# Kernel optimization log

Hardware: AMD Instinct MI355X
Metric: run time of the kernel (lower is better)

The kernel has to match this reference:

```python
import jax, jax.numpy as jnp
import numpy as np

NTOKEN, NINP, NHID, B = 32000, 1024, 1024, 4096


def _rev_lstm_cell(x, c, h, W, b):
    # W: [6, H, D_in+H], b: [6, H]. Gates 0..2 use concat(x,h); 3..5 use concat(x,new_c).
    cat1 = jnp.concatenate([x, h], axis=-1)                      # [B, D+H]
    z1 = jnp.einsum('bd,khd->bkh', cat1, W[:3]) + b[:3]          # [B, 3, H]
    f = jax.nn.sigmoid(z1[:, 0])
    i = jax.nn.sigmoid(z1[:, 1])
    c_ = jnp.tanh(z1[:, 2])
    new_c = (f * c + i * c_) * 0.5
    cat2 = jnp.concatenate([x, new_c], axis=-1)
    z2 = jnp.einsum('bd,khd->bkh', cat2, W[3:]) + b[3:]          # [B, 3, H]
    u = jax.nn.sigmoid(z2[:, 0])
    r = jax.nn.sigmoid(z2[:, 1])
    h_ = jnp.tanh(z2[:, 2])
    new_h = (r * h + u * h_) * 0.5
    return new_h, new_c


def setup_inputs() -> dict:
    key = jax.random.key(0)
    ks = jax.random.split(key, 8)
    gain = 0.01
    def xav(k, shape):
        fan_out, fan_in = shape[-2], shape[-1]
        a = gain * np.sqrt(6.0 / (fan_in + fan_out))
        return jax.random.uniform(k, shape, jnp.float32, -a, a)
    return {
        'input_ids': jax.random.randint(ks[0], (B,), 0, NTOKEN),
        'c1': jnp.zeros((B, NHID), jnp.float32),
        'h1': jnp.zeros((B, NHID), jnp.float32),
        'c2': jnp.zeros((B, NHID), jnp.float32),
        'h2': jnp.zeros((B, NHID), jnp.float32),
        'emb_W': jax.random.uniform(ks[1], (NTOKEN, NINP), jnp.float32, -0.1, 0.1),
        'cell1_W': xav(ks[2], (6, NHID, NINP + NHID)),
        'cell1_b': jnp.zeros((6, NHID), jnp.float32),
        'cell2_W': xav(ks[3], (6, NHID, NHID + NHID)),
        'cell2_b': jnp.zeros((6, NHID), jnp.float32),
        'dec_W': jax.random.uniform(ks[4], (NTOKEN, NHID), jnp.float32, -0.1, 0.1),
        'dec_b': jnp.zeros((NTOKEN,), jnp.float32),
    }


def reference(input_ids, c1, h1, c2, h2, emb_W, cell1_W, cell1_b, cell2_W, cell2_b, dec_W, dec_b):
    emb = emb_W[input_ids]                                       # [B, NINP]
    h1n, c1n = _rev_lstm_cell(emb, c1, h1, cell1_W, cell1_b)
    h2n, c2n = _rev_lstm_cell(h1n, c2, h2, cell2_W, cell2_b)
    decoded = h2n @ dec_W.T + dec_b                              # [B, NTOKEN]
    return decoded, c1n, h1n, c2n, h2n
```

## Files before the change

### kernel.cpp

```cpp
#include <hip/hip_runtime.h>


typedef __attribute__((ext_vector_type(4))) float f32x4;
typedef __attribute__((ext_vector_type(8))) short bf16x8;
typedef __attribute__((ext_vector_type(4))) unsigned short u16x4;
typedef __attribute__((ext_vector_type(4))) int i32x4;

__device__ __forceinline__ unsigned short f2bf(float x) {
  unsigned u = __float_as_uint(x);
  return (unsigned short)((u + 0x7fffu + ((u >> 16) & 1u)) >> 16);
}
__device__ __forceinline__ u16x4 cvt4v(f32x4 v) {
  u16x4 h;
  h[0] = f2bf(v[0]); h[1] = f2bf(v[1]); h[2] = f2bf(v[2]); h[3] = f2bf(v[3]);
  return h;
}
__device__ __forceinline__ float sigf(float x) { return 1.0f / (1.0f + expf(-x)); }

__device__ __forceinline__ void conv_chunk(const float* __restrict__ src,
                                           unsigned short* __restrict__ dst,
                                           long i, long n4) {
  if (i >= n4) return;
  f32x4 v = __builtin_nontemporal_load(reinterpret_cast<const f32x4*>(src) + i);
  reinterpret_cast<u16x4*>(dst)[i] = cvt4v(v);
}

__global__ void fused_pre(const float* __restrict__ W1, unsigned short* __restrict__ cWb1,
                          const float* __restrict__ W2, unsigned short* __restrict__ cWb2,
                          const int* __restrict__ ids, const float* __restrict__ embW,
                          const float* __restrict__ h1, const float* __restrict__ h2,
                          unsigned short* __restrict__ A0, unsigned short* __restrict__ A1,
                          unsigned short* __restrict__ A2) {
  const long n4 = 6L * 1024 * 2048 / 4;
  int b = blockIdx.x;
  int t = threadIdx.x;
  if (b < 12288) {
    conv_chunk(W1, cWb1, (long)b * 256 + t, n4);
  } else if (b < 24576) {
    conv_chunk(W2, cWb2, (long)(b - 12288) * 256 + t, n4);
  } else {
    int r = b - 24576;
    long erow = (long)ids[r] * 1024;
    u16x4 e = cvt4v(reinterpret_cast<const f32x4*>(embW + erow)[t]);
    reinterpret_cast<u16x4*>(A0 + (long)r * 2048)[t] = e;
    reinterpret_cast<u16x4*>(A1 + (long)r * 2048)[t] = e;
    reinterpret_cast<u16x4*>(A0 + (long)r * 2048 + 1024)[t] =
        cvt4v(reinterpret_cast<const f32x4*>(h1 + (long)r * 1024)[t]);
    reinterpret_cast<u16x4*>(A2 + (long)r * 2048 + 1024)[t] =
        cvt4v(reinterpret_cast<const f32x4*>(h2 + (long)r * 1024)[t]);
  }
}

__global__ void quantRow(const float* __restrict__ src, signed char* __restrict__ q,
                         float* __restrict__ scale) {
  int row = blockIdx.x * 4 + (threadIdx.x >> 6);
  int l = threadIdx.x & 63;
  const f32x4* p = reinterpret_cast<const f32x4*>(src + (long)row * 1024);
  f32x4 v[4];
  float m = 0.0f;
#pragma unroll
  for (int i = 0; i < 4; ++i) {
    v[i] = p[l * 4 + i];
#pragma unroll
    for (int j = 0; j < 4; ++j) m = fmaxf(m, fabsf(v[i][j]));
  }
#pragma unroll
  for (int off = 32; off > 0; off >>= 1) m = fmaxf(m, __shfl_xor(m, off));
  float s = (m > 0.0f) ? m * (1.0f / 127.0f) : 1.0f;
  if (l == 0) scale[row] = s;
  float inv = 1.0f / s;
  i32x4 w;
#pragma unroll
  for (int i = 0; i < 4; ++i) {
    int b0 = __float2int_rn(v[i][0] * inv);
    int b1 = __float2int_rn(v[i][1] * inv);
    int b2 = __float2int_rn(v[i][2] * inv);
    int b3 = __float2int_rn(v[i][3] * inv);
    b0 = min(127, max(-127, b0)); b1 = min(127, max(-127, b1));
    b2 = min(127, max(-127, b2)); b3 = min(127, max(-127, b3));
    w[i] = (b0 & 0xff) | ((b1 & 0xff) << 8) | ((b2 & 0xff) << 16) | (b3 << 24);
  }
  *reinterpret_cast<i32x4*>(q + (long)row * 1024 + l * 16) = w;
}

__device__ __forceinline__ void load16(const void* g, void* l) {
  __builtin_amdgcn_global_load_lds((const __attribute__((address_space(1))) unsigned int*)g,
                                   (__attribute__((address_space(3))) unsigned int*)l,
                                   16, 0, 0);
}

#define WAITV(n) do { asm volatile("s_waitcnt vmcnt(" #n ")" ::: "memory");      \
    __builtin_amdgcn_sched_barrier(0); } while (0)
#define BAR() __builtin_amdgcn_s_barrier()
#define SCHED0() __builtin_amdgcn_sched_barrier(0)

__device__ __forceinline__ void superblock(int gx, int gy, int& bx, int& by) {
  const int nwg = gx * gy;
  int bid = blockIdx.y * gx + blockIdx.x;
  const int q = nwg >> 3;
  const int x = bid & 7, j = bid >> 3;
  const int p = x >> 1, half = x & 1;
  const int w0 = (gx + 1) >> 1;
  int byl;
  if ((w0 << 2) == q) {
    bx = half * w0 + (j >> 2);
    byl = j & 3;
  } else {
    if (j < q - 2) { bx = (half ? w0 : 0) + (j >> 2); byl = j & 3; }
    else { bx = w0 - 1; byl = (half ? 2 : 0) + (j - (q - 2)); }
  }
  by = p * 4 + byl;
}

template <int SWAP>
__global__ __launch_bounds__(512, 2) void gemm8f(
    const unsigned short* __restrict__ A,
    const unsigned short* __restrict__ B,
    const float* __restrict__ bias,
    const float* __restrict__ prev,
    float* __restrict__ outf,
    unsigned short* __restrict__ obf1,
    unsigned short* __restrict__ obf2, long obld) {
  __shared__ unsigned short lds[57344];

  int bx, by;
  superblock(gridDim.x, gridDim.y, bx, by);
  const long m0 = (long)by * 256;

  const int tid = threadIdx.x;
  const int lane = tid & 63;
  const int wave = tid >> 6;
  const int wr = wave >> 2;
  const int wc = wave & 3;
  const int lr = lane & 15;
  const int lq = lane >> 4;
  const int kb = lq * 16;

  const int o0 = tid * 16, o1 = tid * 16 + 8192;
  const int q0 = o0 ^ (((o0 >> 7) & 3) << 4);
  const int q1 = o1 ^ (((o1 >> 7) & 3) << 4);
  const char* pa0 = (const char*)(A + (m0 + (q0 >> 6)) * 2048) + (q0 & 63);
  const char* pa1 = (const char*)(A + (m0 + (q1 >> 6)) * 2048) + (q1 & 63);
  const int oB1 = 8192 + (tid & 255) * 16;
  const int qB1 = oB1 ^ (((oB1 >> 7) & 3) << 4);
  const int lrow0 = q0 >> 6, lrow1 = qB1 >> 6;
  const long grow0 = (long)(lrow0 >> 6) * 1024 + bx * 64 + (lrow0 & 63);
  const long grow1 = (long)(lrow1 >> 6) * 1024 + bx * 64 + (lrow1 & 63);
  const char* pb0 = (const char*)(B + grow0 * 2048) + (q0 & 63);
  const char* pb1 = (const char*)(B + grow1 * 2048) + (qB1 & 63);

  const int NT = 32;

#define STG_A(t_, kh_) do { int ko = ((t_) << 7) + ((kh_) << 6);                 \
    char* base_ = (char*)&lds[0] + ((t_) & 1) * 57344;                           \
    char* dst = base_ + ((kh_) ? 28672 : 0);                                     \
    load16(pa0 + ko, dst + o0); load16(pa1 + ko, dst + o1); } while (0)
#define STG_B(t_, kh_) do { int ko = ((t_) << 7) + ((kh_) << 6);                 \
    char* base_ = (char*)&lds[0] + ((t_) & 1) * 57344;                           \
    char* dst = base_ + ((kh_) ? 45056 : 16384);                                 \
    load16(pb0 + ko, dst + o0); load16(pb1 + ko, dst + oB1); } while (0)
#define RDA(dst, bp, soff, ih) do {                                              \
    _Pragma("unroll") for (int i_ = 0; i_ < 4; ++i_) {                           \
      int o_ = (wr * 128 + ((ih) * 4 + i_) * 16 + lr) * 64 + kb;                 \
      o_ ^= ((o_ >> 7) & 3) << 4;                                                \
      dst[i_] = *(const bf16x8*)((bp) + (soff) + o_); } } while (0)
#define RDB(dst, bp, soff) do {                                                  \
    _Pragma("unroll") for (int g_ = 0; g_ < 3; ++g_) {                           \
      int o_ = (g_ * 64 + wc * 16 + lr) * 64 + kb;                               \
      o_ ^= ((o_ >> 7) & 3) << 4;                                                \
      dst[g_] = *(const bf16x8*)((bp) + (soff) + o_); } } while (0)
#define MF12(ar, af_, bf_) do {                                                  \
    _Pragma("unroll") for (int i_ = 0; i_ < 4; ++i_)                             \
    _Pragma("unroll") for (int g_ = 0; g_ < 3; ++g_)                             \
      acc[(ar) + i_][g_] = __builtin_amdgcn_mfma_f32_16x16x32_bf16(              \
          af_[i_], bf_[g_], acc[(ar) + i_][g_], 0, 0, 0); } while (0)

  f32x4 acc[8][3] = {};
  bf16x8 af1[4], af2[4], bfA[3], bfB[3];

  STG_B(0, 0); STG_A(0, 0); STG_B(0, 1); STG_A(0, 1);
  STG_B(1, 0); STG_A(1, 0); STG_B(1, 1);
  WAITV(10);
  BAR();
  {
    const char* b0 = (const char*)&lds[0];
    RDA(af1, b0, 0, 0);
    RDB(bfA, b0, 16384);
  }

  for (int t = 0; t < NT; ++t) {
    const char* base = (const char*)&lds[0] + (t & 1) * 57344;
    const char* baseN = (const char*)&lds[0] + ((t + 1) & 1) * 57344;
    RDA(af2, base, 0, 1);
    if (t + 1 < NT) STG_A(t + 1, 1);
    SCHED0();
    __builtin_amdgcn_s_setprio(1);
    MF12(0, af1, bfA);
    __builtin_amdgcn_s_setprio(0);
    if (t < NT - 1) { WAITV(8); } else { WAITV(0); }
    BAR();
    RDA(af1, base, 28672, 0);
    RDB(bfB, base, 45056);
    if (t + 2 < NT) STG_B(t + 2, 0);
    SCHED0();
    __builtin_amdgcn_s_setprio(1);
    MF12(4, af2, bfA);
    __builtin_amdgcn_s_setprio(0);
    BAR();
    RDA(af2, base, 28672, 1);
    if (t + 2 < NT) STG_A(t + 2, 0);
    SCHED0();
    __builtin_amdgcn_s_setprio(1);
    MF12(0, af1, bfB);
    __builtin_amdgcn_s_setprio(0);
    if (t < NT - 2) { WAITV(8); } else if (t == NT - 2) { WAITV(4); }
    BAR();
    if (t + 1 < NT) {
      RDA(af1, baseN, 0, 0);
      RDB(bfA, baseN, 16384);
    }
    if (t + 2 < NT) STG_B(t + 2, 1);
    SCHED0();
    __builtin_amdgcn_s_setprio(1);
    MF12(4, af2, bfB);
    __builtin_amdgcn_s_setprio(0);
    BAR();
  }

  const long colg = (long)bx * 64 + wc * 16 + lr;
  const float b0v = bias[colg];
  const float b1v = bias[1024 + colg];
  const float b2v = bias[2048 + colg];
#pragma unroll
  for (int i = 0; i < 8; ++i) {
#pragma unroll
    for (int qq = 0; qq < 4; ++qq) {
      long r = m0 + wr * 128 + i * 16 + lq * 4 + qq;
      float z0 = acc[i][0][qq] + b0v;
      float z1 = acc[i][1][qq] + b1v;
      float z2 = acc[i][2][qq] + b2v;
      float zp = SWAP ? z1 : z0;
      float zn = SWAP ? z0 : z1;
      float p = prev[r * 1024 + colg];
      float o = (sigf(zp) * p + sigf(zn) * tanhf(z2)) * 0.5f;
      __builtin_nontemporal_store(o, &outf[r * 1024 + colg]);
      unsigned short ob = f2bf(o);
      obf1[r * obld + colg] = ob;
      if (obf2) obf2[r * obld + colg] = ob;
    }
  }
#undef STG_A
#undef STG_B
#undef RDA
#undef RDB
#undef MF12
}

__global__ __launch_bounds__(512, 2) void gemm8i(
    const signed char* __restrict__ A,
    const signed char* __restrict__ B,
    const float* __restrict__ sA, const float* __restrict__ sW,
    const float* __restrict__ bias, float* __restrict__ C, long ldc) {
  __shared__ unsigned short lds[2][4][8192];

  int bx, by;
  superblock(gridDim.x, gridDim.y, bx, by);
  const long m0 = (long)by * 256;
  const long n0 = (long)bx * 256;

  const int tid = threadIdx.x;
  const int lane = tid & 63;
  const int wave = tid >> 6;
  const int wr = wave >> 2;
  const int wc = wave & 3;
  const int lr = lane & 15;
  const int lq = lane >> 4;
  const int kb = lq * 16;

  const int o0 = tid * 16, o1 = tid * 16 + 8192;
  const int q0 = o0 ^ (((o0 >> 7) & 3) << 4);
  const int q1 = o1 ^ (((o1 >> 7) & 3) << 4);
  const char* pa0 = (const char*)A + (m0 + (q0 >> 6)) * 1024 + (q0 & 63);
  const char* pa1 = (const char*)A + (m0 + (q1 >> 6)) * 1024 + (q1 & 63);
  const char* pb0 = (const char*)B + (n0 + (q0 >> 6)) * 1024 + (q0 & 63);
  const char* pb1 = (const char*)B + (n0 + (q1 >> 6)) * 1024 + (q1 & 63);

  const int NT = 8;

#define STG_A(t_, kh_) do { int ko = ((t_) << 7) + ((kh_) << 6);                 \
    char* d = (char*)&lds[(t_) & 1][(kh_) ? 2 : 0][0];                           \
    load16(pa0 + ko, d + o0); load16(pa1 + ko, d + o1); } while (0)
#define STG_B(t_, kh_) do { int ko = ((t_) << 7) + ((kh_) << 6);                 \
    char* d = (char*)&lds[(t_) & 1][(kh_) ? 3 : 1][0];                           \
    load16(pb0 + ko, d + o0); load16(pb1 + ko, d + o1); } while (0)
#define RDA(dst, bp, soff, ih) do {                                              \
    _Pragma("unroll") for (int i_ = 0; i_ < 4; ++i_) {                           \
      int o_ = (wr * 128 + ((ih) * 4 + i_) * 16 + lr) * 64 + kb;                 \
      o_ ^= ((o_ >> 7) & 3) << 4;                                                \
      dst[i_] = *(const i32x4*)((bp) + (soff) + o_); } } while (0)
#define RDB(dst, bp, soff) do {                                                  \
    _Pragma("unroll") for (int j_ = 0; j_ < 4; ++j_) {                           \
      int o_ = (wc * 64 + j_ * 16 + lr) * 64 + kb;                               \
      o_ ^= ((o_ >> 7) & 3) << 4;                                                \
      dst[j_] = *(const i32x4*)((bp) + (soff) + o_); } } while (0)
#define MF16(ar, af_, bf_) do {                                                  \
    _Pragma("unroll") for (int i_ = 0; i_ < 4; ++i_)                             \
    _Pragma("unroll") for (int j_ = 0; j_ < 4; ++j_)                             \
      acc[(ar) + i_][j_] = __builtin_amdgcn_mfma_i32_16x16x64_i8(                \
          af_[i_], bf_[j_], acc[(ar) + i_][j_], 0, 0, 0); } while (0)

  i32x4 acc[8][4] = {};
  i32x4 af1[4], af2[4], bfA[4], bfB[4];

  STG_B(0, 0); STG_A(0, 0); STG_B(0, 1); STG_A(0, 1);
  STG_B(1, 0); STG_A(1, 0); STG_B(1, 1);
  WAITV(10);
  BAR();
  {
    const char* b0 = (const char*)&lds[0][0][0];
    RDA(af1, b0, 0, 0);
    RDB(bfA, b0, 16384);
  }

  for (int t = 0; t < NT; ++t) {
    const char* base = (const char*)&lds[0][0][0] + (t & 1) * 65536;
    const char* baseN = (const char*)&lds[0][0][0] + ((t + 1) & 1) * 65536;
    RDA(af2, base, 0, 1);
    if (t + 1 < NT) STG_A(t + 1, 1);
    SCHED0();
    __builtin_amdgcn_s_setprio(1);
    MF16(0, af1, bfA);
    __builtin_amdgcn_s_setprio(0);
    if (t < NT - 1) { WAITV(8); } else { WAITV(0); }
    BAR();
    RDA(af1, base, 32768, 0);
    RDB(bfB, base, 49152);
    if (t + 2 < NT) STG_B(t + 2, 0);
    SCHED0();
    __builtin_amdgcn_s_setprio(1);
    MF16(4, af2, bfA);
    __builtin_amdgcn_s_setprio(0);
    BAR();
    RDA(af2, base, 32768, 1);
    if (t + 2 < NT) STG_A(t + 2, 0);
    SCHED0();
    __builtin_amdgcn_s_setprio(1);
    MF16(0, af1, bfB);
    __builtin_amdgcn_s_setprio(0);
    if (t < NT - 2) { WAITV(8); } else if (t == NT - 2) { WAITV(4); }
    BAR();
    if (t + 1 < NT) {
      RDA(af1, baseN, 0, 0);
      RDB(bfA, baseN, 16384);
    }
    if (t + 2 < NT) STG_B(t + 2, 1);
    SCHED0();
    __builtin_amdgcn_s_setprio(1);
    MF16(4, af2, bfB);
    __builtin_amdgcn_s_setprio(0);
    BAR();
  }

  int* Tw = (int*)&lds[0][0][0] + wave * 2176;
  f32x4 bv4 = *(const f32x4*)&bias[n0 + wc * 64 + lr * 4];
  f32x4 sw4 = *(const f32x4*)&sW[n0 + wc * 64 + lr * 4];
#pragma unroll
  for (int i = 0; i < 8; ++i) {
    int* T = Tw + (i & 1) * 1088;
#pragma unroll
    for (int jj = 0; jj < 4; ++jj)
#pragma unroll
      for (int qq = 0; qq < 4; ++qq)
        T[(lq * 4 + qq) * 68 + jj * 16 + lr] = acc[i][jj][qq];
#pragma unroll
    for (int s = 0; s < 4; ++s) {
      i32x4 iv = *(const i32x4*)&T[(s * 4 + lq) * 68 + lr * 4];
      long row = m0 + wr * 128 + i * 16 + s * 4 + lq;
      float sa = sA[row];
      f32x4 v;
      v[0] = (float)iv[0]; v[1] = (float)iv[1]; v[2] = (float)iv[2]; v[3] = (float)iv[3];
      v = v * (sa * sw4) + bv4;
      __builtin_nontemporal_store(v, (f32x4*)&C[row * ldc + n0 + wc * 64 + lr * 4]);
    }
  }
#undef STG_A
#undef STG_B
#undef RDA
#undef RDB
#undef MF16
}

extern "C" void kernel_launch(void* const* d_in, const int* in_sizes, int n_in,
                              void* d_out, int out_size, void* d_ws, size_t ws_size,
                              hipStream_t stream) {
  const int*   ids  = (const int*)d_in[0];
  const float* c1   = (const float*)d_in[1];
  const float* h1   = (const float*)d_in[2];
  const float* c2   = (const float*)d_in[3];
  const float* h2   = (const float*)d_in[4];
  const float* embW = (const float*)d_in[5];
  const float* W1   = (const float*)d_in[6];
  const float* b1   = (const float*)d_in[7];
  const float* W2   = (const float*)d_in[8];
  const float* b2   = (const float*)d_in[9];
  const float* decW = (const float*)d_in[10];
  const float* decb = (const float*)d_in[11];
  float* out = (float*)d_out;

  char* ws = (char*)d_ws;
  unsigned short* A0   = (unsigned short*)(ws);
  unsigned short* A1   = (unsigned short*)(ws + 16777216L);
  unsigned short* A2   = (unsigned short*)(ws + 33554432L);
  unsigned short* cWb1 = (unsigned short*)(ws + 50331648L);
  unsigned short* cWb2 = (unsigned short*)(ws + 75497472L);
  signed char*    qW   = (signed char*)(ws + 50331648L);
  signed char*    qA   = (signed char*)(ws + 83886080L);
  float*          sA   = (float*)(ws + 88080384L);
  float*          sW   = (float*)(ws + 88096768L);

  float* out_dec = out;
  float* out_c1  = out + 131072000L;
  float* out_h1  = out_c1 + 4194304L;
  float* out_c2  = out_h1 + 4194304L;
  float* out_h2  = out_c2 + 4194304L;

  dim3 blk(256), gblk(512);
  dim3 gcell(16, 16);

  fused_pre<<<dim3(28672), blk, 0, stream>>>(W1, cWb1, W2, cWb2, ids, embW, h1, h2,
                                             A0, A1, A2);

  gemm8f<0><<<gcell, gblk, 0, stream>>>(A0, cWb1, b1, c1,
                                        out_c1, A1 + 1024, nullptr, 2048);
  gemm8f<1><<<gcell, gblk, 0, stream>>>(A1, cWb1 + 3072L * 2048, b1 + 3072, h1,
                                        out_h1, A2, A0, 2048);
  gemm8f<0><<<gcell, gblk, 0, stream>>>(A2, cWb2, b2, c2,
                                        out_c2, A0 + 1024, nullptr, 2048);
  gemm8f<1><<<gcell, gblk, 0, stream>>>(A0, cWb2 + 3072L * 2048, b2 + 3072, h2,
                                        out_h2, A1, nullptr, 1024);

  quantRow<<<dim3(1024), blk, 0, stream>>>(out_h2, qA, sA);
  quantRow<<<dim3(8000), blk, 0, stream>>>(decW, qW, sW);
  {
    dim3 g(125, 16);
    gemm8i<<<g, gblk, 0, stream>>>(qA, qW, sA, sW, decb, out_dec, 32000);
  }
}
```

Measured before the change: 513.1 us.

## Quantize LSTM cell GEMMs to int8 with per-row scales

Switches the four cell GEMMs from bf16 MFMA to int8 MFMA (16x16x64), quantizing the weights per row and the concatenated activations per row in separate qcat kernels. The decoder weight quantization moves into the fused preprocessing kernel. The goal is to halve operand bytes and double MFMA throughput. The cost is three extra small quantize launches between GEMMs and int8 accuracy loss in the recurrent cell outputs.

```diff
diff --git a/kernel.cpp b/kernel.cpp
--- a/kernel.cpp
+++ b/kernel.cpp
@@ -2,53 +2,120 @@
 
 
 typedef __attribute__((ext_vector_type(4))) float f32x4;
-typedef __attribute__((ext_vector_type(8))) short bf16x8;
 typedef __attribute__((ext_vector_type(4))) unsigned short u16x4;
 typedef __attribute__((ext_vector_type(4))) int i32x4;
 
-__device__ __forceinline__ unsigned short f2bf(float x) {
-  unsigned u = __float_as_uint(x);
-  return (unsigned short)((u + 0x7fffu + ((u >> 16) & 1u)) >> 16);
-}
-__device__ __forceinline__ u16x4 cvt4v(f32x4 v) {
-  u16x4 h;
-  h[0] = f2bf(v[0]); h[1] = f2bf(v[1]); h[2] = f2bf(v[2]); h[3] = f2bf(v[3]);
-  return h;
-}
 __device__ __forceinline__ float sigf(float x) { return 1.0f / (1.0f + expf(-x)); }
 
-__device__ __forceinline__ void conv_chunk(const float* __restrict__ src,
-                                           unsigned short* __restrict__ dst,
-                                           long i, long n4) {
-  if (i >= n4) return;
-  f32x4 v = __builtin_nontemporal_load(reinterpret_cast<const f32x4*>(src) + i);
-  reinterpret_cast<u16x4*>(dst)[i] = cvt4v(v);
-}
-
-__global__ void fused_pre(const float* __restrict__ W1, unsigned short* __restrict__ cWb1,
-                          const float* __restrict__ W2, unsigned short* __restrict__ cWb2,
+__device__ __forceinline__ int pack4(f32x4 v, float inv) {
+  int b0 = __float2int_rn(v[0] * inv);
+  int b1 = __float2int_rn(v[1] * inv);
+  int b2 = __float2int_rn(v[2] * inv);
+  int b3 = __float2int_rn(v[3] * inv);
+  b0 = min(127, max(-127, b0)); b1 = min(127, max(-127, b1));
+  b2 = min(127, max(-127, b2)); b3 = min(127, max(-127, b3));
+  return (b0 & 0xff) | ((b1 & 0xff) << 8) | ((b2 & 0xff) << 16) | (b3 << 24);
+}
+__device__ __forceinline__ float amax4(f32x4 v, float m) {
+  m = fmaxf(m, fabsf(v[0])); m = fmaxf(m, fabsf(v[1]));
+  m = fmaxf(m, fabsf(v[2])); m = fmaxf(m, fabsf(v[3]));
+  return m;
+}
+__device__ __forceinline__ float wavemax(float m) {
+#pragma unroll
+  for (int off = 32; off > 0; off >>= 1) m = fmaxf(m, __shfl_xor(m, off));
+  return m;
+}
+
+__global__ void fused_pre(const float* __restrict__ W1, const float* __restrict__ W2,
+                          signed char* __restrict__ qWc, float* __restrict__ sWc,
+                          const float* __restrict__ decW, signed char* __restrict__ qWd,
+                          float* __restrict__ sWd,
                           const int* __restrict__ ids, const float* __restrict__ embW,
-                          const float* __restrict__ h1, const float* __restrict__ h2,
-                          unsigned short* __restrict__ A0, unsigned short* __restrict__ A1,
-                          unsigned short* __restrict__ A2) {
-  const long n4 = 6L * 1024 * 2048 / 4;
+                          const float* __restrict__ h1,
+                          signed char* __restrict__ qA0, float* __restrict__ sA0) {
   int b = blockIdx.x;
-  int t = threadIdx.x;
-  if (b < 12288) {
-    conv_chunk(W1, cWb1, (long)b * 256 + t, n4);
-  } else if (b < 24576) {
-    conv_chunk(W2, cWb2, (long)(b - 12288) * 256 + t, n4);
+  int l = threadIdx.x & 63;
+  int wv = threadIdx.x >> 6;
+  if (b < 3072) {
+    int row = b * 4 + wv;
+    const float* src = (row < 6144) ? (W1 + (long)row * 2048)
+                                    : (W2 + (long)(row - 6144) * 2048);
+    const f32x4* p = reinterpret_cast<const f32x4*>(src);
+    f32x4 v[8];
+    float m = 0.0f;
+#pragma unroll
+    for (int i = 0; i < 8; ++i) { v[i] = p[l + 64 * i]; m = amax4(v[i], m); }
+    m = wavemax(m);
+    float s = (m > 0.0f) ? m * (1.0f / 127.0f) : 1.0f;
+    if (l == 0) sWc[row] = s;
+    float inv = 1.0f / s;
+    int* q = reinterpret_cast<int*>(qWc + (long)row * 2048);
+#pragma unroll
+    for (int i = 0; i < 8; ++i) q[l + 64 * i] = pack4(v[i], inv);
+  } else if (b < 11072) {
+    int row = (b - 3072) * 4 + wv;
+    const f32x4* p = reinterpret_cast<const f32x4*>(decW + (long)row * 1024);
+    f32x4 v[4];
+    float m = 0.0f;
+#pragma unroll
+    for (int i = 0; i < 4; ++i) { v[i] = p[l * 4 + i]; m = amax4(v[i], m); }
+    m = wavemax(m);
+    float s = (m > 0.0f) ? m * (1.0f / 127.0f) : 1.0f;
+    if (l == 0) sWd[row] = s;
+    float inv = 1.0f / s;
+    i32x4 w;
+#pragma unroll
+    for (int i = 0; i < 4; ++i) w[i] = pack4(v[i], inv);
+    *reinterpret_cast<i32x4*>(qWd + (long)row * 1024 + l * 16) = w;
   } else {
-    int r = b - 24576;
-    long erow = (long)ids[r] * 1024;
-    u16x4 e = cvt4v(reinterpret_cast<const f32x4*>(embW + erow)[t]);
-    reinterpret_cast<u16x4*>(A0 + (long)r * 2048)[t] = e;
-    reinterpret_cast<u16x4*>(A1 + (long)r * 2048)[t] = e;
-    reinterpret_cast<u16x4*>(A0 + (long)r * 2048 + 1024)[t] =
-        cvt4v(reinterpret_cast<const f32x4*>(h1 + (long)r * 1024)[t]);
-    reinterpret_cast<u16x4*>(A2 + (long)r * 2048 + 1024)[t] =
-        cvt4v(reinterpret_cast<const f32x4*>(h2 + (long)r * 1024)[t]);
-  }
+    int row = (b - 11072) * 4 + wv;
+    const f32x4* p1 = reinterpret_cast<const f32x4*>(embW + (long)ids[row] * 1024);
+    const f32x4* p2 = reinterpret_cast<const f32x4*>(h1 + (long)row * 1024);
+    f32x4 v1[4], v2[4];
+    float m = 0.0f;
+#pragma unroll
+    for (int i = 0; i < 4; ++i) {
+      v1[i] = p1[l * 4 + i]; m = amax4(v1[i], m);
+      v2[i] = p2[l * 4 + i]; m = amax4(v2[i], m);
+    }
+    m = wavemax(m);
+    float s = (m > 0.0f) ? m * (1.0f / 127.0f) : 1.0f;
+    if (l == 0) sA0[row] = s;
+    float inv = 1.0f / s;
+    i32x4 w1, w2;
+#pragma unroll
+    for (int i = 0; i < 4; ++i) { w1[i] = pack4(v1[i], inv); w2[i] = pack4(v2[i], inv); }
+    *reinterpret_cast<i32x4*>(qA0 + (long)row * 2048 + l * 16) = w1;
+    *reinterpret_cast<i32x4*>(qA0 + (long)row * 2048 + 1024 + l * 16) = w2;
+  }
+}
+
+__global__ void qcat(const float* __restrict__ src1, const int* __restrict__ ids,
+                     const float* __restrict__ embW, const float* __restrict__ src2,
+                     signed char* __restrict__ q, float* __restrict__ scale) {
+  int row = blockIdx.x * 4 + (threadIdx.x >> 6);
+  int l = threadIdx.x & 63;
+  const f32x4* p1 = ids
+      ? reinterpret_cast<const f32x4*>(embW + (long)ids[row] * 1024)
+      : reinterpret_cast<const f32x4*>(src1 + (long)row * 1024);
+  const f32x4* p2 = reinterpret_cast<const f32x4*>(src2 + (long)row * 1024);
+  f32x4 v1[4], v2[4];
+  float m = 0.0f;
+#pragma unroll
+  for (int i = 0; i < 4; ++i) {
+    v1[i] = p1[l * 4 + i]; m = amax4(v1[i], m);
+    v2[i] = p2[l * 4 + i]; m = amax4(v2[i], m);
+  }
+  m = wavemax(m);
+  float s = (m > 0.0f) ? m * (1.0f / 127.0f) : 1.0f;
+  if (l == 0) scale[row] = s;
+  float inv = 1.0f / s;
+  i32x4 w1, w2;
+#pragma unroll
+  for (int i = 0; i < 4; ++i) { w1[i] = pack4(v1[i], inv); w2[i] = pack4(v2[i], inv); }
+  *reinterpret_cast<i32x4*>(q + (long)row * 2048 + l * 16) = w1;
+  *reinterpret_cast<i32x4*>(q + (long)row * 2048 + 1024 + l * 16) = w2;
 }
 
 __global__ void quantRow(const float* __restrict__ src, signed char* __restrict__ q,
@@ -59,27 +126,14 @@
   f32x4 v[4];
   float m = 0.0f;
 #pragma unroll
-  for (int i = 0; i < 4; ++i) {
-    v[i] = p[l * 4 + i];
-#pragma unroll
-    for (int j = 0; j < 4; ++j) m = fmaxf(m, fabsf(v[i][j]));
-  }
-#pragma unroll
-  for (int off = 32; off > 0; off >>= 1) m = fmaxf(m, __shfl_xor(m, off));
+  for (int i = 0; i < 4; ++i) { v[i] = p[l * 4 + i]; m = amax4(v[i], m); }
+  m = wavemax(m);
   float s = (m > 0.0f) ? m * (1.0f / 127.0f) : 1.0f;
   if (l == 0) scale[row] = s;
   float inv = 1.0f / s;
   i32x4 w;
 #pragma unroll
-  for (int i = 0; i < 4; ++i) {
-    int b0 = __float2int_rn(v[i][0] * inv);
-    int b1 = __float2int_rn(v[i][1] * inv);
-    int b2 = __float2int_rn(v[i][2] * inv);
-    int b3 = __float2int_rn(v[i][3] * inv);
-    b0 = min(127, max(-127, b0)); b1 = min(127, max(-127, b1));
-    b2 = min(127, max(-127, b2)); b3 = min(127, max(-127, b3));
-    w[i] = (b0 & 0xff) | ((b1 & 0xff) << 8) | ((b2 & 0xff) << 16) | (b3 << 24);
-  }
+  for (int i = 0; i < 4; ++i) w[i] = pack4(v[i], inv);
   *reinterpret_cast<i32x4*>(q + (long)row * 1024 + l * 16) = w;
 }
 
@@ -113,15 +167,13 @@
 }
 
 template <int SWAP>
-__global__ __launch_bounds__(512, 2) void gemm8f(
-    const unsigned short* __restrict__ A,
-    const unsigned short* __restrict__ B,
+__global__ __launch_bounds__(512, 2) void gemm8q(
+    const signed char* __restrict__ A, const float* __restrict__ sAv,
+    const signed char* __restrict__ B, const float* __restrict__ swb,
     const float* __restrict__ bias,
     const float* __restrict__ prev,
-    float* __restrict__ outf,
-    unsigned short* __restrict__ obf1,
-    unsigned short* __restrict__ obf2, long obld) {
-  __shared__ unsigned short lds[57344];
+    float* __restrict__ outf) {
+  __shared__ unsigned char lds[114688];
 
   int bx, by;
   superblock(gridDim.x, gridDim.y, bx, by);
@@ -139,17 +191,17 @@
   const int o0 = tid * 16, o1 = tid * 16 + 8192;
   const int q0 = o0 ^ (((o0 >> 7) & 3) << 4);
   const int q1 = o1 ^ (((o1 >> 7) & 3) << 4);
-  const char* pa0 = (const char*)(A + (m0 + (q0 >> 6)) * 2048) + (q0 & 63);
-  const char* pa1 = (const char*)(A + (m0 + (q1 >> 6)) * 2048) + (q1 & 63);
+  const char* pa0 = (const char*)A + (m0 + (q0 >> 6)) * 2048 + (q0 & 63);
+  const char* pa1 = (const char*)A + (m0 + (q1 >> 6)) * 2048 + (q1 & 63);
   const int oB1 = 8192 + (tid & 255) * 16;
   const int qB1 = oB1 ^ (((oB1 >> 7) & 3) << 4);
   const int lrow0 = q0 >> 6, lrow1 = qB1 >> 6;
   const long grow0 = (long)(lrow0 >> 6) * 1024 + bx * 64 + (lrow0 & 63);
   const long grow1 = (long)(lrow1 >> 6) * 1024 + bx * 64 + (lrow1 & 63);
-  const char* pb0 = (const char*)(B + grow0 * 2048) + (q0 & 63);
-  const char* pb1 = (const char*)(B + grow1 * 2048) + (qB1 & 63);
-
-  const int NT = 32;
+  const char* pb0 = (const char*)B + grow0 * 2048 + (q0 & 63);
+  const char* pb1 = (const char*)B + grow1 * 2048 + (qB1 & 63);
+
+  const int NT = 16;
 
 #define STG_A(t_, kh_) do { int ko = ((t_) << 7) + ((kh_) << 6);                 \
     char* base_ = (char*)&lds[0] + ((t_) & 1) * 57344;                           \
@@ -163,20 +215,20 @@
     _Pragma("unroll") for (int i_ = 0; i_ < 4; ++i_) {                           \
       int o_ = (wr * 128 + ((ih) * 4 + i_) * 16 + lr) * 64 + kb;                 \
       o_ ^= ((o_ >> 7) & 3) << 4;                                                \
-      dst[i_] = *(const bf16x8*)((bp) + (soff) + o_); } } while (0)
+      dst[i_] = *(const i32x4*)((bp) + (soff) + o_); } } while (0)
 #define RDB(dst, bp, soff) do {                                                  \
     _Pragma("unroll") for (int g_ = 0; g_ < 3; ++g_) {                           \
       int o_ = (g_ * 64 + wc * 16 + lr) * 64 + kb;                               \
       o_ ^= ((o_ >> 7) & 3) << 4;                                                \
-      dst[g_] = *(const bf16x8*)((bp) + (soff) + o_); } } while (0)
+      dst[g_] = *(const i32x4*)((bp) + (soff) + o_); } } while (0)
 #define MF12(ar, af_, bf_) do {                                                  \
     _Pragma("unroll") for (int i_ = 0; i_ < 4; ++i_)                             \
     _Pragma("unroll") for (int g_ = 0; g_ < 3; ++g_)                             \
-      acc[(ar) + i_][g_] = __builtin_amdgcn_mfma_f32_16x16x32_bf16(              \
+      acc[(ar) + i_][g_] = __builtin_amdgcn_mfma_i32_16x16x64_i8(                \
           af_[i_], bf_[g_], acc[(ar) + i_][g_], 0, 0, 0); } while (0)
 
-  f32x4 acc[8][3] = {};
-  bf16x8 af1[4], af2[4], bfA[3], bfB[3];
+  i32x4 acc[8][3] = {};
+  i32x4 af1[4], af2[4], bfA[3], bfB[3];
 
   STG_B(0, 0); STG_A(0, 0); STG_B(0, 1); STG_A(0, 1);
   STG_B(1, 0); STG_A(1, 0); STG_B(1, 1);
@@ -231,22 +283,23 @@
   const float b0v = bias[colg];
   const float b1v = bias[1024 + colg];
   const float b2v = bias[2048 + colg];
+  const float s0 = swb[colg];
+  const float s1 = swb[1024 + colg];
+  const float s2 = swb[2048 + colg];
 #pragma unroll
   for (int i = 0; i < 8; ++i) {
 #pragma unroll
     for (int qq = 0; qq < 4; ++qq) {
       long r = m0 + wr * 128 + i * 16 + lq * 4 + qq;
-      float z0 = acc[i][0][qq] + b0v;
-      float z1 = acc[i][1][qq] + b1v;
-      float z2 = acc[i][2][qq] + b2v;
+      float sa = sAv[r];
+      float z0 = (float)acc[i][0][qq] * (sa * s0) + b0v;
+      float z1 = (float)acc[i][1][qq] * (sa * s1) + b1v;
+      float z2 = (float)acc[i][2][qq] * (sa * s2) + b2v;
       float zp = SWAP ? z1 : z0;
       float zn = SWAP ? z0 : z1;
       float p = prev[r * 1024 + colg];
       float o = (sigf(zp) * p + sigf(zn) * tanhf(z2)) * 0.5f;
       __builtin_nontemporal_store(o, &outf[r * 1024 + colg]);
-      unsigned short ob = f2bf(o);
-      obf1[r * obld + colg] = ob;
-      if (obf2) obf2[r * obld + colg] = ob;
     }
   }
 #undef STG_A
@@ -408,15 +461,18 @@
   float* out = (float*)d_out;
 
   char* ws = (char*)d_ws;
-  unsigned short* A0   = (unsigned short*)(ws);
-  unsigned short* A1   = (unsigned short*)(ws + 16777216L);
-  unsigned short* A2   = (unsigned short*)(ws + 33554432L);
-  unsigned short* cWb1 = (unsigned short*)(ws + 50331648L);
-  unsigned short* cWb2 = (unsigned short*)(ws + 75497472L);
-  signed char*    qW   = (signed char*)(ws + 50331648L);
-  signed char*    qA   = (signed char*)(ws + 83886080L);
-  float*          sA   = (float*)(ws + 88080384L);
-  float*          sW   = (float*)(ws + 88096768L);
+  signed char* qA0 = (signed char*)(ws);
+  signed char* qA1 = (signed char*)(ws + 8388608L);
+  signed char* qA2 = (signed char*)(ws + 16777216L);
+  signed char* qWc = (signed char*)(ws + 25165824L);
+  signed char* qWd = (signed char*)(ws + 50331648L);
+  signed char* qAd = (signed char*)(ws + 83099648L);
+  float* sA0 = (float*)(ws + 87293952L);
+  float* sA1 = (float*)(ws + 87310336L);
+  float* sA2 = (float*)(ws + 87326720L);
+  float* sWc = (float*)(ws + 87343104L);
+  float* sWd = (float*)(ws + 87392256L);
+  float* sAd = (float*)(ws + 87520256L);
 
   float* out_dec = out;
   float* out_c1  = out + 131072000L;
@@ -426,23 +482,25 @@
 
   dim3 blk(256), gblk(512);
   dim3 gcell(16, 16);
-
-  fused_pre<<<dim3(28672), blk, 0, stream>>>(W1, cWb1, W2, cWb2, ids, embW, h1, h2,
-                                             A0, A1, A2);
-
-  gemm8f<0><<<gcell, gblk, 0, stream>>>(A0, cWb1, b1, c1,
-                                        out_c1, A1 + 1024, nullptr, 2048);
-  gemm8f<1><<<gcell, gblk, 0, stream>>>(A1, cWb1 + 3072L * 2048, b1 + 3072, h1,
-                                        out_h1, A2, A0, 2048);
-  gemm8f<0><<<gcell, gblk, 0, stream>>>(A2, cWb2, b2, c2,
-                                        out_c2, A0 + 1024, nullptr, 2048);
-  gemm8f<1><<<gcell, gblk, 0, stream>>>(A0, cWb2 + 3072L * 2048, b2 + 3072, h2,
-                                        out_h2, A1, nullptr, 1024);
-
-  quantRow<<<dim3(1024), blk, 0, stream>>>(out_h2, qA, sA);
-  quantRow<<<dim3(8000), blk, 0, stream>>>(decW, qW, sW);
+  const long WROW = 2048;
+
+  fused_pre<<<dim3(12096), blk, 0, stream>>>(W1, W2, qWc, sWc, decW, qWd, sWd,
+                                             ids, embW, h1, qA0, sA0);
+
+  gemm8q<0><<<gcell, gblk, 0, stream>>>(qA0, sA0, qWc, sWc, b1, c1, out_c1);
+  qcat<<<dim3(1024), blk, 0, stream>>>(nullptr, ids, embW, out_c1, qA1, sA1);
+  gemm8q<1><<<gcell, gblk, 0, stream>>>(qA1, sA1, qWc + 3072L * WROW, sWc + 3072,
+                                        b1 + 3072, h1, out_h1);
+  qcat<<<dim3(1024), blk, 0, stream>>>(out_h1, nullptr, nullptr, h2, qA2, sA2);
+  gemm8q<0><<<gcell, gblk, 0, stream>>>(qA2, sA2, qWc + 6144L * WROW, sWc + 6144,
+                                        b2, c2, out_c2);
+  qcat<<<dim3(1024), blk, 0, stream>>>(out_h1, nullptr, nullptr, out_c2, qA0, sA0);
+  gemm8q<1><<<gcell, gblk, 0, stream>>>(qA0, sA0, qWc + 9216L * WROW, sWc + 9216,
+                                        b2 + 3072, h2, out_h2);
+
+  quantRow<<<dim3(1024), blk, 0, stream>>>(out_h2, qAd, sAd);
   {
     dim3 g(125, 16);
-    gemm8i<<<g, gblk, 0, stream>>>(qA, qW, sA, sW, decb, out_dec, 32000);
-  }
-}
+    gemm8i<<<g, gblk, 0, stream>>>(qAd, qWd, sAd, sWd, decb, out_dec, 32000);
+  }
+}
```

After: 437.2 us. 14.8% less time.
